# Kernel tuning notes

Hardware: AMD Instinct MI355X
Metric: run time of the kernel (lower is better)

The kernel has to match this reference:

```python
import jax, jax.numpy as jnp
import numpy as np

DIM = 2048
N_HEADS = 32
N_KV_HEADS = 8
HEAD_DIM = DIM // N_HEADS  # 64
N_REP = N_HEADS // N_KV_HEADS  # 4
ROPE_BASE = 10000.0


def _rope_cos_sin(seq_len, head_dim, dtype):
    inv_freq = 1.0 / (ROPE_BASE ** (jnp.arange(0, head_dim, 2, dtype=jnp.float32) / head_dim))
    freqs = jnp.arange(seq_len, dtype=jnp.float32)[:, None] * inv_freq[None, :]  # [S, hd/2]
    return jnp.cos(freqs).astype(dtype), jnp.sin(freqs).astype(dtype)


def _apply_rope(x, cos, sin):
    # x: [B, S, H, hd]; cos/sin: [S, hd/2]
    x1, x2 = jnp.split(x, 2, axis=-1)
    c = cos[None, :, None, :]
    s = sin[None, :, None, :]
    return jnp.concatenate([x1 * c - x2 * s, x1 * s + x2 * c], axis=-1)


def setup_inputs() -> dict:
    key = jax.random.key(0)
    ks = jax.random.split(key, 5)
    B, S = 2, 2048
    x = jax.random.normal(ks[0], (B, S, DIM), dtype=jnp.float32)
    scale = 1.0 / np.sqrt(DIM)
    wq = jax.random.normal(ks[1], (DIM, DIM), dtype=jnp.float32) * scale
    wk = jax.random.normal(ks[2], (N_KV_HEADS * HEAD_DIM, DIM), dtype=jnp.float32) * scale
    wv = jax.random.normal(ks[3], (N_KV_HEADS * HEAD_DIM, DIM), dtype=jnp.float32) * scale
    wo = jax.random.normal(ks[4], (DIM, DIM), dtype=jnp.float32) * scale
    return {"x": x, "wq": wq, "wk": wk, "wv": wv, "wo": wo}


def reference(x, wq, wk, wv, wo):
    B, S, D = x.shape
    # projections (nn.Linear: y = x @ W.T)
    xq = (x @ wq.T).reshape(B, S, N_HEADS, HEAD_DIM)
    xk = (x @ wk.T).reshape(B, S, N_KV_HEADS, HEAD_DIM)
    xv = (x @ wv.T).reshape(B, S, N_KV_HEADS, HEAD_DIM)

    cos, sin = _rope_cos_sin(S, HEAD_DIM, x.dtype)
    xq = _apply_rope(xq, cos, sin)
    xk = _apply_rope(xk, cos, sin)

    # GQA: repeat kv heads
    keys = jnp.repeat(xk, N_REP, axis=2)    # [B, S, H, hd]
    values = jnp.repeat(xv, N_REP, axis=2)

    scores = jnp.einsum('bqhd,bkhd->bhqk', xq, keys) / np.sqrt(HEAD_DIM)
    causal = jnp.tril(jnp.ones((S, S), dtype=bool))
    scores = jnp.where(causal[None, None, :, :], scores, jnp.finfo(scores.dtype).min)
    probs = jax.nn.softmax(scores, axis=-1)
    out = jnp.einsum('bhqk,bkhd->bqhd', probs, values).reshape(B, S, D)
    return out @ wo.T  # dropout in eval mode == identity
```

## Files before the change

kernel.cpp:

```cpp
#include <hip/hip_runtime.h>

typedef __attribute__((ext_vector_type(8))) short bf16x8;
typedef __attribute__((ext_vector_type(4))) float f32x4;
typedef __attribute__((ext_vector_type(4))) unsigned short u16x4;

#define GPTR(p) (const __attribute__((address_space(1))) void*)(p)
#define LPTR(p) (__attribute__((address_space(3))) void*)(p)

static __device__ __forceinline__ unsigned short f2bf(float f) {
  union { float f; unsigned int u; } x; x.f = f;
  unsigned int u = x.u;
  unsigned int r = (u + 0x7fffu + ((u >> 16) & 1u)) >> 16;
  return (unsigned short)r;
}
static __device__ __forceinline__ float bf2f(unsigned short h) {
  union { unsigned int u; float f; } x; x.u = ((unsigned int)h) << 16;
  return x.f;
}
static __device__ __forceinline__ f32x4 f32x4_zero() {
  f32x4 z = {0.f, 0.f, 0.f, 0.f}; return z;
}
static __device__ __forceinline__ unsigned int cvt_pk_bf16(float lo, float hi) {
  unsigned int r;
  asm("v_cvt_pk_bf16_f32 %0, %1, %2" : "=v"(r) : "v"(lo), "v"(hi));
  return r;
}

__global__ void rope_table_kernel(float* __restrict__ costab, float* __restrict__ sintab) {
  int i = blockIdx.x * blockDim.x + threadIdx.x;
  int s = i >> 5, d = i & 31;
  float invf = exp2f(-(float)d * (13.287712379549449f / 32.0f));
  float a = (float)s * invf;
  costab[i] = cosf(a);
  sintab[i] = sinf(a);
}

__global__ void f32_to_bf16(const float* __restrict__ src, unsigned short* __restrict__ dst, int n4) {
  int stride = gridDim.x * blockDim.x;
  for (int i = blockIdx.x * blockDim.x + threadIdx.x; i < n4; i += stride) {
    float4 v = ((const float4*)src)[i];
    u16x4 o;
    o.x = f2bf(v.x); o.y = f2bf(v.y); o.z = f2bf(v.z); o.w = f2bf(v.w);
    *(u16x4*)(dst + (size_t)i * 4) = o;
  }
}

template<int FM, int OUT_BF16>
__global__ __launch_bounds__(512, 2) void gemm8p(const unsigned short* __restrict__ A,
                                                 const unsigned short* __restrict__ B,
                                                 void* __restrict__ Cv,
                                                 int M, int N, int K, int nbx) {
  constexpr int BM = FM * 32;
  constexpr int MH = FM / 2;
  constexpr int ABYTES = BM * 128;
  constexpr int BBYTES = 256 * 128;
  __shared__ __align__(16) char lds_all[2 * ABYTES + 2 * BBYTES];
  char* lsA = lds_all;
  char* lsB = lds_all + 2 * ABYTES;

  const int tid = threadIdx.x;
  const int wave = tid >> 6, lane = tid & 63;
  const int fq = lane >> 4, fr = lane & 15;
  const int wr = wave >> 2, wc = wave & 3;

  const int nwg = gridDim.x;
  const int q8 = nwg >> 3;
  const int sw = (blockIdx.x & 7) * q8 + (blockIdx.x >> 3);
  const int by = sw / nbx;
  const int bx = sw - by * nbx;
  const int m0 = by * BM, n0 = bx * 256;

  const int arow = tid >> 3;
  const int scol = (((tid & 7) ^ (arow & 7)) << 4);

#define STAGE_A(bufv, kt, h)                                                                  \
  do {                                                                                        \
    const char* src_ = (const char*)A + ((size_t)(m0 + (h) * 128 + arow) * K + (kt) * 64) * 2 + scol; \
    char* dst_ = lsA + (bufv) * ABYTES + (h) * 16384 + tid * 16;                              \
    __builtin_amdgcn_global_load_lds(GPTR(src_), LPTR(dst_), 16, 0, 0);                       \
    __builtin_amdgcn_global_load_lds(GPTR(src_ + (size_t)64 * K * 2), LPTR(dst_ + 8192), 16, 0, 0); \
  } while (0)
#define STAGE_B(bufv, kt, h)                                                                  \
  do {                                                                                        \
    const char* src_ = (const char*)B + ((size_t)(n0 + (h) * 128 + arow) * K + (kt) * 64) * 2 + scol; \
    char* dst_ = lsB + (bufv) * BBYTES + (h) * 16384 + tid * 16;                              \
    __builtin_amdgcn_global_load_lds(GPTR(src_), LPTR(dst_), 16, 0, 0);                       \
    __builtin_amdgcn_global_load_lds(GPTR(src_ + (size_t)64 * K * 2), LPTR(dst_ + 8192), 16, 0, 0); \
  } while (0)

  f32x4 acc[FM][4];
#pragma unroll
  for (int i = 0; i < FM; ++i)
#pragma unroll
    for (int j = 0; j < 4; ++j) acc[i][j] = f32x4_zero();

#define PHASE(p)                                                                              \
  do {                                                                                        \
    constexpr int mh = (p) >> 1, nh = (p) & 1;                                                \
    bf16x8 af[MH][2], bfv[2][2];                                                              \
    _Pragma("unroll") for (int m = 0; m < MH; ++m) {                                          \
      const int rowA = wr * FM * 16 + mh * MH * 16 + m * 16 + fr;                             \
      const char* pa = lsA + buf * ABYTES + (rowA >> 7) * 16384 + (rowA & 127) * 128;         \
      const int sz = (rowA & 7) << 4;                                                         \
      af[m][0] = *(const bf16x8*)(pa + ((fq * 16) ^ sz));                                     \
      af[m][1] = *(const bf16x8*)(pa + ((64 + fq * 16) ^ sz));                                \
    }                                                                                         \
    _Pragma("unroll") for (int n = 0; n < 2; ++n) {                                           \
      const int rowB = wc * 64 + nh * 32 + n * 16 + fr;                                       \
      const char* pb = lsB + buf * BBYTES + (rowB >> 7) * 16384 + (rowB & 127) * 128;         \
      const int sz = (rowB & 7) << 4;                                                         \
      bfv[n][0] = *(const bf16x8*)(pb + ((fq * 16) ^ sz));                                    \
      bfv[n][1] = *(const bf16x8*)(pb + ((64 + fq * 16) ^ sz));                               \
    }                                                                                         \
    asm volatile("s_waitcnt lgkmcnt(0)" ::: "memory");                                        \
    __builtin_amdgcn_sched_barrier(0);                                                        \
    __builtin_amdgcn_s_setprio(1);                                                            \
    _Pragma("unroll") for (int m = 0; m < MH; ++m)                                            \
      _Pragma("unroll") for (int n = 0; n < 2; ++n) {                                         \
        acc[mh * MH + m][nh * 2 + n] =                                                        \
            __builtin_amdgcn_mfma_f32_16x16x32_bf16(af[m][0], bfv[n][0], acc[mh * MH + m][nh * 2 + n], 0, 0, 0); \
        acc[mh * MH + m][nh * 2 + n] =                                                        \
            __builtin_amdgcn_mfma_f32_16x16x32_bf16(af[m][1], bfv[n][1], acc[mh * MH + m][nh * 2 + n], 0, 0, 0); \
      }                                                                                       \
    __builtin_amdgcn_s_setprio(0);                                                            \
  } while (0)

  const int NT = K >> 6;

  STAGE_A(0, 0, 0);
  if constexpr (FM == 8) STAGE_A(0, 0, 1);
  STAGE_B(0, 0, 0);
  STAGE_B(0, 0, 1);
  asm volatile("s_waitcnt vmcnt(0)" ::: "memory");
  __builtin_amdgcn_s_barrier();

  int buf = 0;
  for (int t = 0; t < NT; ++t) {
    const bool hn = (t + 1) < NT;
    if (hn) {
      STAGE_A(buf ^ 1, t + 1, 0);
      asm volatile("s_waitcnt vmcnt(2)" ::: "memory");
    } else {
      asm volatile("s_waitcnt vmcnt(0)" ::: "memory");
    }
    __builtin_amdgcn_s_barrier();
    PHASE(0);
    __builtin_amdgcn_s_barrier();
    if (hn) {
      if constexpr (FM == 8) STAGE_A(buf ^ 1, t + 1, 1);
      else                   STAGE_B(buf ^ 1, t + 1, 0);
    }
    PHASE(1);
    __builtin_amdgcn_s_barrier();
    if (hn) {
      if constexpr (FM == 8) STAGE_B(buf ^ 1, t + 1, 0);
      else                   STAGE_B(buf ^ 1, t + 1, 1);
    }
    PHASE(2);
    __builtin_amdgcn_s_barrier();
    if (hn) {
      if constexpr (FM == 8) STAGE_B(buf ^ 1, t + 1, 1);
    }
    PHASE(3);
    __builtin_amdgcn_s_barrier();
    buf ^= 1;
  }

#pragma unroll
  for (int i = 0; i < FM; ++i) {
    const int row = m0 + wr * FM * 16 + i * 16 + fq * 4;
#pragma unroll
    for (int j = 0; j < 4; ++j) {
      const int col = n0 + wc * 64 + j * 16 + fr;
#pragma unroll
      for (int v = 0; v < 4; ++v) {
        if (OUT_BF16) ((unsigned short*)Cv)[(size_t)(row + v) * N + col] = f2bf(acc[i][j][v]);
        else          ((float*)Cv)[(size_t)(row + v) * N + col] = acc[i][j][v];
      }
    }
  }
#undef STAGE_A
#undef STAGE_B
#undef PHASE
}

__global__ void rope_kernel(unsigned short* __restrict__ qkv,
                            const float* __restrict__ costab,
                            const float* __restrict__ sintab) {
  int idx = blockIdx.x * blockDim.x + threadIdx.x;
  if (idx >= 4096 * 1280) return;
  int row = idx / 1280;
  int p = idx - row * 1280;
  int s = row & 2047;
  int col, d; bool isq;
  if (p < 1024) { isq = true;  d = p & 31; col = (p >> 5) * 64 + d; }
  else { isq = false; int pk = p - 1024; d = pk & 31; col = 2048 + (pk >> 5) * 64 + d; }
  float c = costab[s * 32 + d], sn = sintab[s * 32 + d];
  unsigned short* base = qkv + (size_t)row * 3072;
  float x1 = bf2f(base[col]), x2 = bf2f(base[col + 32]);
  float o1 = x1 * c - x2 * sn;
  float o2 = x1 * sn + x2 * c;
  if (isq) { o1 *= 0.18033688011112042f; o2 *= 0.18033688011112042f; }
  base[col] = f2bf(o1);
  base[col + 32] = f2bf(o2);
}

__global__ __launch_bounds__(512, 4) void flash_attn(const unsigned short* __restrict__ qkv,
                                                     unsigned short* __restrict__ out) {
  __shared__ __align__(16) char K_sh[2 * 8192];
  __shared__ __align__(16) char V_sh[2 * 8192];
  __shared__ __align__(16) char P_sh[8 * 4096];

  const int tid = threadIdx.x;
  const int wave = tid >> 6, lane = tid & 63;
  const int fq = lane >> 4, fr = lane & 15;
  const int id = blockIdx.x;
  const int w = id >> 8, c = id & 255;
  const int hb = c & 63;
  const int h = hb & 31, b = hb >> 5;
  const int qhalf = c >> 6;
  const int qt = w ? qhalf : 7 - qhalf;
  const int kvh = h >> 2;
  const int q0 = qt * 256;
  const int wq0 = q0 + wave * 32;
  char* Pw = P_sh + wave * 4096;

  bf16x8 qreg[2][2];
#pragma unroll
  for (int qf = 0; qf < 2; ++qf)
#pragma unroll
    for (int kk = 0; kk < 2; ++kk)
      qreg[qf][kk] = *(const bf16x8*)(qkv + (size_t)(b * 2048 + wq0 + qf * 16 + fr) * 3072
                                      + h * 64 + kk * 32 + fq * 8);

  f32x4 o_acc[4][2];
  float m_run[2], l_run[2];
#pragma unroll
  for (int dc = 0; dc < 4; ++dc) { o_acc[dc][0] = f32x4_zero(); o_acc[dc][1] = f32x4_zero(); }
  m_run[0] = m_run[1] = -1e30f;
  l_run[0] = l_run[1] = 0.f;

  const char* kgbase = (const char*)qkv + (size_t)(b * 2048) * 6144 + 4096 + kvh * 128;
  const unsigned short* vgbase = qkv + (size_t)(b * 2048) * 3072 + 2560 + kvh * 64;
  const int nsteps = (q0 + 256) >> 6;

  const int vk2 = (tid >> 3) << 1;
  const int vc0 = (tid & 7) << 3;
  const int kt = tid - 256;

  {
    if (wave < 4) {
      bf16x8 vv0 = *(const bf16x8*)(vgbase + (size_t)vk2 * 3072 + vc0);
      bf16x8 vv1 = *(const bf16x8*)(vgbase + (size_t)(vk2 + 1) * 3072 + vc0);
#pragma unroll
      for (int j = 0; j < 8; ++j) {
        const int d = vc0 + j;
        const int G = ((d & 7) ^ (d >> 3)) & 7;
        unsigned int w2 = ((unsigned int)(unsigned short)vv0[j]) |
                          (((unsigned int)(unsigned short)vv1[j]) << 16);
        *(unsigned int*)(V_sh + (d << 7) + ((vk2 << 1) ^ (G << 4))) = w2;
      }
    } else {
#pragma unroll
      for (int ld = 0; ld < 2; ++ld) {
        const int row = (kt >> 3) + (ld << 5);
        const int cb = ((kt & 7) << 4) ^ ((row & 7) << 4);
        __builtin_amdgcn_global_load_lds(GPTR(kgbase + (size_t)row * 6144 + cb),
                                         LPTR(K_sh + kt * 16 + ld * 4096), 16, 0, 0);
      }
    }
  }
  __syncthreads();

  int buf = 0;
  for (int st = 0; st < nsteps; ++st) {
    const int k0 = st << 6;
    const bool has_next = (st + 1) < nsteps;
    bf16x8 vv0, vv1;
    if (has_next) {
      const int k0n = k0 + 64;
      if (wave < 4) {
        vv0 = *(const bf16x8*)(vgbase + (size_t)(k0n + vk2) * 3072 + vc0);
        vv1 = *(const bf16x8*)(vgbase + (size_t)(k0n + vk2 + 1) * 3072 + vc0);
      } else {
        char* Kn = K_sh + (buf ^ 1) * 8192;
#pragma unroll
        for (int ld = 0; ld < 2; ++ld) {
          const int row = (kt >> 3) + (ld << 5);
          const int cb = ((kt & 7) << 4) ^ ((row & 7) << 4);
          __builtin_amdgcn_global_load_lds(GPTR(kgbase + (size_t)(k0n + row) * 6144 + cb),
                                           LPTR(Kn + kt * 16 + ld * 4096), 16, 0, 0);
        }
      }
    }

    if (k0 <= wq0 + 31) {
      const char* Kb = K_sh + buf * 8192;
      const char* Vb = V_sh + buf * 8192;
      f32x4 s[2][4];
#pragma unroll
      for (int qf = 0; qf < 2; ++qf)
#pragma unroll
        for (int kf = 0; kf < 4; ++kf) s[qf][kf] = f32x4_zero();
#pragma unroll
      for (int kf = 0; kf < 4; ++kf) {
        const int krow = kf * 16 + fr;
        const int swz = (krow & 7) << 4;
        bf16x8 ka = *(const bf16x8*)(Kb + krow * 128 + ((fq * 16) ^ swz));
        bf16x8 kb = *(const bf16x8*)(Kb + krow * 128 + ((64 + fq * 16) ^ swz));
#pragma unroll
        for (int qf = 0; qf < 2; ++qf) {
          s[qf][kf] = __builtin_amdgcn_mfma_f32_16x16x32_bf16(ka, qreg[qf][0], s[qf][kf], 0, 0, 0);
          s[qf][kf] = __builtin_amdgcn_mfma_f32_16x16x32_bf16(kb, qreg[qf][1], s[qf][kf], 0, 0, 0);
        }
      }
      if (k0 + 63 > wq0) {
#pragma unroll
        for (int qf = 0; qf < 2; ++qf) {
          const int q = wq0 + qf * 16 + fr;
#pragma unroll
          for (int kf = 0; kf < 4; ++kf)
#pragma unroll
            for (int v = 0; v < 4; ++v) {
              const int key = k0 + kf * 16 + fq * 4 + v;
              if (key > q) s[qf][kf][v] = -1e30f;
            }
        }
      }
#pragma unroll
      for (int qf = 0; qf < 2; ++qf) {
        float t = s[qf][0][0];
#pragma unroll
        for (int kf = 0; kf < 4; ++kf)
#pragma unroll
          for (int v = 0; v < 4; ++v) t = fmaxf(t, s[qf][kf][v]);
        t = fmaxf(t, __shfl_xor(t, 16));
        t = fmaxf(t, __shfl_xor(t, 32));
        const float mo = m_run[qf];
        const float mn = fmaxf(mo, t);
        const float sc = __builtin_amdgcn_exp2f(mo - mn);
        m_run[qf] = mn;
        float ps = 0.f;
#pragma unroll
        for (int kf = 0; kf < 4; ++kf)
#pragma unroll
          for (int v = 0; v < 4; ++v) {
            const float p = __builtin_amdgcn_exp2f(s[qf][kf][v] - mn);
            s[qf][kf][v] = p;
            ps += p;
          }
        ps += __shfl_xor(ps, 16);
        ps += __shfl_xor(ps, 32);
        l_run[qf] = l_run[qf] * sc + ps;
#pragma unroll
        for (int dc = 0; dc < 4; ++dc) o_acc[dc][qf] *= sc;
        const int r = qf * 16 + fr;
        const int rswz = (r & 7) << 4;
#pragma unroll
        for (int kf = 0; kf < 4; ++kf) {
          uint2 w2;
          w2.x = cvt_pk_bf16(s[qf][kf][0], s[qf][kf][1]);
          w2.y = cvt_pk_bf16(s[qf][kf][2], s[qf][kf][3]);
          *(uint2*)(Pw + r * 128 + ((kf * 32 + fq * 8) ^ rswz)) = w2;
        }
      }
      asm volatile("s_waitcnt lgkmcnt(0)" ::: "memory");
      __builtin_amdgcn_sched_barrier(0);
      const int fswz = (fr & 7) << 4;
#pragma unroll
      for (int kk = 0; kk < 2; ++kk) {
        bf16x8 pa0 = *(const bf16x8*)(Pw + fr * 128 + ((kk * 64 + fq * 16) ^ fswz));
        bf16x8 pa1 = *(const bf16x8*)(Pw + (16 + fr) * 128 + ((kk * 64 + fq * 16) ^ fswz));
#pragma unroll
        for (int dc = 0; dc < 4; ++dc) {
          const int d = dc * 16 + fr;
          const int G = ((d & 7) ^ (d >> 3)) & 7;
          bf16x8 vt = *(const bf16x8*)(Vb + d * 128 + ((kk * 64 + fq * 16) ^ (G << 4)));
          o_acc[dc][0] = __builtin_amdgcn_mfma_f32_16x16x32_bf16(vt, pa0, o_acc[dc][0], 0, 0, 0);
          o_acc[dc][1] = __builtin_amdgcn_mfma_f32_16x16x32_bf16(vt, pa1, o_acc[dc][1], 0, 0, 0);
        }
      }
    }

    if (has_next && wave < 4) {
      char* Vn = V_sh + (buf ^ 1) * 8192;
#pragma unroll
      for (int j = 0; j < 8; ++j) {
        const int d = vc0 + j;
        const int G = ((d & 7) ^ (d >> 3)) & 7;
        unsigned int w2 = ((unsigned int)(unsigned short)vv0[j]) |
                          (((unsigned int)(unsigned short)vv1[j]) << 16);
        *(unsigned int*)(Vn + (d << 7) + ((vk2 << 1) ^ (G << 4))) = w2;
      }
    }
    __syncthreads();
    buf ^= 1;
  }

#pragma unroll
  for (int qf = 0; qf < 2; ++qf) {
    const float inv = 1.0f / l_run[qf];
    const size_t row = (size_t)(b * 2048 + wq0 + qf * 16 + fr);
#pragma unroll
    for (int dc = 0; dc < 4; ++dc) {
      u16x4 o;
#pragma unroll
      for (int v = 0; v < 4; ++v) o[v] = f2bf(o_acc[dc][qf][v] * inv);
      *(u16x4*)(out + row * 2048 + h * 64 + dc * 16 + fq * 4) = o;
    }
  }
}

extern "C" void kernel_launch(void* const* d_in, const int* in_sizes, int n_in,
                              void* d_out, int out_size, void* d_ws, size_t ws_size,
                              hipStream_t stream) {
  (void)in_sizes; (void)n_in; (void)out_size; (void)ws_size;
  const float* x  = (const float*)d_in[0];
  const float* wq = (const float*)d_in[1];
  const float* wk = (const float*)d_in[2];
  const float* wv = (const float*)d_in[3];
  const float* wo = (const float*)d_in[4];

  char* wsb = (char*)d_ws;
  unsigned short* xb     = (unsigned short*)(wsb);
  unsigned short* attn_o = xb;
  unsigned short* wqkvb  = (unsigned short*)(wsb + 16777216);
  unsigned short* wob    = (unsigned short*)(wsb + 29360128);
  unsigned short* qkv    = (unsigned short*)(wsb + 37748736);
  float* costab          = (float*)(wsb + 62914560);
  float* sintab          = (float*)(wsb + 63176704);

  rope_table_kernel<<<256, 256, 0, stream>>>(costab, sintab);

  f32_to_bf16<<<2048, 256, 0, stream>>>(x,  xb,                 8388608 / 4);
  f32_to_bf16<<<1024, 256, 0, stream>>>(wq, wqkvb,              4194304 / 4);
  f32_to_bf16<<<256,  256, 0, stream>>>(wk, wqkvb + 4194304,    1048576 / 4);
  f32_to_bf16<<<256,  256, 0, stream>>>(wv, wqkvb + 5242880,    1048576 / 4);
  f32_to_bf16<<<1024, 256, 0, stream>>>(wo, wob,                4194304 / 4);

  gemm8p<8, 1><<<192, 512, 0, stream>>>(xb, wqkvb, (void*)qkv, 4096, 3072, 2048, 12);

  rope_kernel<<<20480, 256, 0, stream>>>(qkv, costab, sintab);

  flash_attn<<<512, 512, 0, stream>>>(qkv, attn_o);

  gemm8p<4, 0><<<256, 512, 0, stream>>>(attn_o, wob, d_out, 4096, 2048, 2048, 8);
}
```

Before: 288.7 us.

## Use lazy softmax rescaling, tree reductions, and reorder block-to-tile mapping

Online softmax now rescales the running max, sum and output accumulators only when some row's new max exceeds the old one by more than a threshold (checked wave-wide). This skips the per-tile exp and accumulator multiply in most iterations. Max and sum reductions are rewritten as balanced trees to shorten dependency chains. The block index mapping changes to put q-tiles innermost in descending order rather than the previous paired heavy/light interleave, which may change load balance across the causal triangle. Exponentials can reach up to about 2^11.5 before rescaling, which is safe in fp32 but trades some bf16 P precision.

```diff
diff --git a/kernel.cpp b/kernel.cpp
--- a/kernel.cpp
+++ b/kernel.cpp
@@ -215,11 +215,9 @@
   const int wave = tid >> 6, lane = tid & 63;
   const int fq = lane >> 4, fr = lane & 15;
   const int id = blockIdx.x;
-  const int w = id >> 8, c = id & 255;
-  const int hb = c & 63;
-  const int h = hb & 31, b = hb >> 5;
-  const int qhalf = c >> 6;
-  const int qt = w ? qhalf : 7 - qhalf;
+  const int qt = 7 - (id & 7);
+  const int h = (id >> 3) & 31;
+  const int b = id >> 8;
   const int kvh = h >> 2;
   const int q0 = qt * 256;
   const int wq0 = q0 + wave * 32;
@@ -327,33 +325,45 @@
             }
         }
       }
+      float pm[2];
 #pragma unroll
       for (int qf = 0; qf < 2; ++qf) {
-        float t = s[qf][0][0];
-#pragma unroll
-        for (int kf = 0; kf < 4; ++kf)
-#pragma unroll
-          for (int v = 0; v < 4; ++v) t = fmaxf(t, s[qf][kf][v]);
+        float a0 = fmaxf(fmaxf(s[qf][0][0], s[qf][0][1]), fmaxf(s[qf][0][2], s[qf][0][3]));
+        float a1 = fmaxf(fmaxf(s[qf][1][0], s[qf][1][1]), fmaxf(s[qf][1][2], s[qf][1][3]));
+        float a2 = fmaxf(fmaxf(s[qf][2][0], s[qf][2][1]), fmaxf(s[qf][2][2], s[qf][2][3]));
+        float a3 = fmaxf(fmaxf(s[qf][3][0], s[qf][3][1]), fmaxf(s[qf][3][2], s[qf][3][3]));
+        float t = fmaxf(fmaxf(a0, a1), fmaxf(a2, a3));
         t = fmaxf(t, __shfl_xor(t, 16));
         t = fmaxf(t, __shfl_xor(t, 32));
-        const float mo = m_run[qf];
-        const float mn = fmaxf(mo, t);
-        const float sc = __builtin_amdgcn_exp2f(mo - mn);
-        m_run[qf] = mn;
-        float ps = 0.f;
+        pm[qf] = t;
+      }
+      if (__any(fmaxf(pm[0] - m_run[0], pm[1] - m_run[1]) > 11.5f)) {
+#pragma unroll
+        for (int qf = 0; qf < 2; ++qf) {
+          const float mn = fmaxf(m_run[qf], pm[qf]);
+          const float sc = __builtin_amdgcn_exp2f(m_run[qf] - mn);
+          m_run[qf] = mn;
+          l_run[qf] *= sc;
+#pragma unroll
+          for (int dc = 0; dc < 4; ++dc) o_acc[dc][qf] *= sc;
+        }
+      }
+#pragma unroll
+      for (int qf = 0; qf < 2; ++qf) {
+        const float mn = m_run[qf];
 #pragma unroll
         for (int kf = 0; kf < 4; ++kf)
 #pragma unroll
-          for (int v = 0; v < 4; ++v) {
-            const float p = __builtin_amdgcn_exp2f(s[qf][kf][v] - mn);
-            s[qf][kf][v] = p;
-            ps += p;
-          }
+          for (int v = 0; v < 4; ++v)
+            s[qf][kf][v] = __builtin_amdgcn_exp2f(s[qf][kf][v] - mn);
+        float b0 = (s[qf][0][0] + s[qf][0][1]) + (s[qf][0][2] + s[qf][0][3]);
+        float b1 = (s[qf][1][0] + s[qf][1][1]) + (s[qf][1][2] + s[qf][1][3]);
+        float b2 = (s[qf][2][0] + s[qf][2][1]) + (s[qf][2][2] + s[qf][2][3]);
+        float b3 = (s[qf][3][0] + s[qf][3][1]) + (s[qf][3][2] + s[qf][3][3]);
+        float ps = (b0 + b1) + (b2 + b3);
         ps += __shfl_xor(ps, 16);
         ps += __shfl_xor(ps, 32);
-        l_run[qf] = l_run[qf] * sc + ps;
-#pragma unroll
-        for (int dc = 0; dc < 4; ++dc) o_acc[dc][qf] *= sc;
+        l_run[qf] += ps;
         const int r = qf * 16 + fr;
         const int rswz = (r & 7) << 4;
 #pragma unroll
```

After: 271.8 us. 5.9% less time.

## Keep attention probabilities in registers via lane permutes instead of LDS round-trip

Applied to the files above, without the earlier changes.

Drops the per-wave shared-memory P buffer. The softmax probabilities are now rearranged from the QK^T accumulator layout into the PV MFMA operand layout using permlane32_swap and xor-16 shuffles. This removes the LDS writes, the wait and the reads on every key tile, and frees 32KB of LDS, which may allow more resident blocks. It also changes the block-to-tile mapping to a plain qt/h/b decode, with causal tiles reversed so the heaviest run first.

```diff
diff --git a/kernel.cpp b/kernel.cpp
--- a/kernel.cpp
+++ b/kernel.cpp
@@ -3,6 +3,7 @@
 typedef __attribute__((ext_vector_type(8))) short bf16x8;
 typedef __attribute__((ext_vector_type(4))) float f32x4;
 typedef __attribute__((ext_vector_type(4))) unsigned short u16x4;
+typedef __attribute__((ext_vector_type(2))) unsigned int u32x2;
 
 #define GPTR(p) (const __attribute__((address_space(1))) void*)(p)
 #define LPTR(p) (__attribute__((address_space(3))) void*)(p)
@@ -209,21 +210,18 @@
                                                      unsigned short* __restrict__ out) {
   __shared__ __align__(16) char K_sh[2 * 8192];
   __shared__ __align__(16) char V_sh[2 * 8192];
-  __shared__ __align__(16) char P_sh[8 * 4096];
 
   const int tid = threadIdx.x;
   const int wave = tid >> 6, lane = tid & 63;
   const int fq = lane >> 4, fr = lane & 15;
+  const int q1 = fq & 1;
   const int id = blockIdx.x;
-  const int w = id >> 8, c = id & 255;
-  const int hb = c & 63;
-  const int h = hb & 31, b = hb >> 5;
-  const int qhalf = c >> 6;
-  const int qt = w ? qhalf : 7 - qhalf;
+  const int qt = 7 - (id & 7);
+  const int h = (id >> 3) & 31;
+  const int b = id >> 8;
   const int kvh = h >> 2;
   const int q0 = qt * 256;
   const int wq0 = q0 + wave * 32;
-  char* Pw = P_sh + wave * 4096;
 
   bf16x8 qreg[2][2];
 #pragma unroll
@@ -354,30 +352,37 @@
         l_run[qf] = l_run[qf] * sc + ps;
 #pragma unroll
         for (int dc = 0; dc < 4; ++dc) o_acc[dc][qf] *= sc;
-        const int r = qf * 16 + fr;
-        const int rswz = (r & 7) << 4;
-#pragma unroll
-        for (int kf = 0; kf < 4; ++kf) {
-          uint2 w2;
-          w2.x = cvt_pk_bf16(s[qf][kf][0], s[qf][kf][1]);
-          w2.y = cvt_pk_bf16(s[qf][kf][2], s[qf][kf][3]);
-          *(uint2*)(Pw + r * 128 + ((kf * 32 + fq * 8) ^ rswz)) = w2;
+      }
+#pragma unroll
+      for (int kk = 0; kk < 2; ++kk) {
+        bf16x8 pb[2];
+#pragma unroll
+        for (int qf = 0; qf < 2; ++qf) {
+          unsigned int u0w0 = cvt_pk_bf16(s[qf][2 * kk][0],     s[qf][2 * kk][1]);
+          unsigned int u0w1 = cvt_pk_bf16(s[qf][2 * kk][2],     s[qf][2 * kk][3]);
+          unsigned int u1w0 = cvt_pk_bf16(s[qf][2 * kk + 1][0], s[qf][2 * kk + 1][1]);
+          unsigned int u1w1 = cvt_pk_bf16(s[qf][2 * kk + 1][2], s[qf][2 * kk + 1][3]);
+          u32x2 s0 = __builtin_amdgcn_permlane32_swap(u0w0, u1w0, false, false);
+          u32x2 s1 = __builtin_amdgcn_permlane32_swap(u0w1, u1w1, false, false);
+          const unsigned int a0 = s0.x, b0 = s0.y, a1 = s1.x, b1 = s1.y;
+          const unsigned int ra0 = (unsigned int)__shfl_xor((int)a0, 16);
+          const unsigned int rb0 = (unsigned int)__shfl_xor((int)b0, 16);
+          const unsigned int ra1 = (unsigned int)__shfl_xor((int)a1, 16);
+          const unsigned int rb1 = (unsigned int)__shfl_xor((int)b1, 16);
+          union { unsigned int u[4]; bf16x8 v; } P;
+          P.u[0] = q1 ? rb0 : a0;
+          P.u[1] = q1 ? rb1 : a1;
+          P.u[2] = q1 ? b0 : ra0;
+          P.u[3] = q1 ? b1 : ra1;
+          pb[qf] = P.v;
         }
-      }
-      asm volatile("s_waitcnt lgkmcnt(0)" ::: "memory");
-      __builtin_amdgcn_sched_barrier(0);
-      const int fswz = (fr & 7) << 4;
-#pragma unroll
-      for (int kk = 0; kk < 2; ++kk) {
-        bf16x8 pa0 = *(const bf16x8*)(Pw + fr * 128 + ((kk * 64 + fq * 16) ^ fswz));
-        bf16x8 pa1 = *(const bf16x8*)(Pw + (16 + fr) * 128 + ((kk * 64 + fq * 16) ^ fswz));
 #pragma unroll
         for (int dc = 0; dc < 4; ++dc) {
           const int d = dc * 16 + fr;
           const int G = ((d & 7) ^ (d >> 3)) & 7;
           bf16x8 vt = *(const bf16x8*)(Vb + d * 128 + ((kk * 64 + fq * 16) ^ (G << 4)));
-          o_acc[dc][0] = __builtin_amdgcn_mfma_f32_16x16x32_bf16(vt, pa0, o_acc[dc][0], 0, 0, 0);
-          o_acc[dc][1] = __builtin_amdgcn_mfma_f32_16x16x32_bf16(vt, pa1, o_acc[dc][1], 0, 0, 0);
+          o_acc[dc][0] = __builtin_amdgcn_mfma_f32_16x16x32_bf16(vt, pb[0], o_acc[dc][0], 0, 0, 0);
+          o_acc[dc][1] = __builtin_amdgcn_mfma_f32_16x16x32_bf16(vt, pb[1], o_acc[dc][1], 0, 0, 0);
         }
       }
     }
```

After: 349.7 us. 1.21x slower.

## Fuse RoPE into QKV GEMM epilogue and merge conversion kernels

Applied to the files above, without the earlier changes.

Applies rotary embedding and the query scale directly in the QKV GEMM epilogue using an interleaved cos/sin table, which removes the separate rope kernel and its extra read-modify-write pass over qkv. The five fp32-to-bf16 conversion launches are merged into one kernel. The flash attention grid moves to a 3D layout with a plain reversed q-tile order, replacing the old balanced pairing of heavy and light tiles. The epilogue rounds to bf16 only once after rotation, which slightly changes numerics, and the new attention block order may change load balance.

```diff
diff --git a/kernel.cpp b/kernel.cpp
--- a/kernel.cpp
+++ b/kernel.cpp
@@ -26,30 +26,41 @@
   return r;
 }
 
-__global__ void rope_table_kernel(float* __restrict__ costab, float* __restrict__ sintab) {
+__global__ void rope_table_kernel(float2* __restrict__ ctab) {
   int i = blockIdx.x * blockDim.x + threadIdx.x;
   int s = i >> 5, d = i & 31;
   float invf = exp2f(-(float)d * (13.287712379549449f / 32.0f));
   float a = (float)s * invf;
-  costab[i] = cosf(a);
-  sintab[i] = sinf(a);
-}
-
-__global__ void f32_to_bf16(const float* __restrict__ src, unsigned short* __restrict__ dst, int n4) {
-  int stride = gridDim.x * blockDim.x;
-  for (int i = blockIdx.x * blockDim.x + threadIdx.x; i < n4; i += stride) {
-    float4 v = ((const float4*)src)[i];
+  ctab[i] = make_float2(cosf(a), sinf(a));
+}
+
+__global__ void convert_all(const float* __restrict__ x,  const float* __restrict__ wq,
+                            const float* __restrict__ wk, const float* __restrict__ wv,
+                            const float* __restrict__ wo,
+                            unsigned short* __restrict__ xb,
+                            unsigned short* __restrict__ wqkvb,
+                            unsigned short* __restrict__ wob) {
+  const int stride = gridDim.x * blockDim.x;
+  for (int i = blockIdx.x * blockDim.x + threadIdx.x; i < 4718592; i += stride) {
+    const float* src; unsigned short* dst; int off;
+    if (i < 2097152)      { src = x;  dst = xb;              off = i; }
+    else if (i < 3145728) { src = wq; dst = wqkvb;           off = i - 2097152; }
+    else if (i < 3407872) { src = wk; dst = wqkvb + 4194304; off = i - 3145728; }
+    else if (i < 3670016) { src = wv; dst = wqkvb + 5242880; off = i - 3407872; }
+    else                  { src = wo; dst = wob;             off = i - 3670016; }
+    float4 v = ((const float4*)src)[off];
     u16x4 o;
     o.x = f2bf(v.x); o.y = f2bf(v.y); o.z = f2bf(v.z); o.w = f2bf(v.w);
-    *(u16x4*)(dst + (size_t)i * 4) = o;
-  }
-}
-
-template<int FM, int OUT_BF16>
+    *(u16x4*)(dst + (size_t)off * 4) = o;
+  }
+}
+
+template<int FM, int OUT_BF16, int ROPE>
 __global__ __launch_bounds__(512, 2) void gemm8p(const unsigned short* __restrict__ A,
                                                  const unsigned short* __restrict__ B,
                                                  void* __restrict__ Cv,
-                                                 int M, int N, int K, int nbx) {
+                                                 int M, int N, int K, int nbx,
+                                                 const float2* __restrict__ ctab) {
   constexpr int BM = FM * 32;
   constexpr int MH = FM / 2;
   constexpr int ABYTES = BM * 128;
@@ -166,43 +177,51 @@
     buf ^= 1;
   }
 
-#pragma unroll
-  for (int i = 0; i < FM; ++i) {
-    const int row = m0 + wr * FM * 16 + i * 16 + fq * 4;
-#pragma unroll
-    for (int j = 0; j < 4; ++j) {
-      const int col = n0 + wc * 64 + j * 16 + fr;
-#pragma unroll
-      for (int v = 0; v < 4; ++v) {
-        if (OUT_BF16) ((unsigned short*)Cv)[(size_t)(row + v) * N + col] = f2bf(acc[i][j][v]);
-        else          ((float*)Cv)[(size_t)(row + v) * N + col] = acc[i][j][v];
+  if constexpr (ROPE) {
+    const int colbase = n0 + wc * 64 + fr;
+#pragma unroll
+    for (int i = 0; i < FM; ++i) {
+      const int row = m0 + wr * FM * 16 + i * 16 + fq * 4;
+      const int s0 = row & 2047;
+#pragma unroll
+      for (int j = 0; j < 2; ++j) {
+        const int col = colbase + j * 16;
+        const bool rot = col < 2560;
+        const float scale = (col < 2048) ? 0.18033688011112042f : 1.0f;
+        const int dp = col & 63;
+#pragma unroll
+        for (int v = 0; v < 4; ++v) {
+          const float a  = acc[i][j][v];
+          const float b2 = acc[i][j + 2][v];
+          float o1 = a, o2 = b2;
+          if (rot) {
+            const float2 cs = ctab[(s0 + v) * 32 + dp];
+            o1 = (a * cs.x - b2 * cs.y) * scale;
+            o2 = (a * cs.y + b2 * cs.x) * scale;
+          }
+          ((unsigned short*)Cv)[(size_t)(row + v) * N + col]      = f2bf(o1);
+          ((unsigned short*)Cv)[(size_t)(row + v) * N + col + 32] = f2bf(o2);
+        }
+      }
+    }
+  } else {
+#pragma unroll
+    for (int i = 0; i < FM; ++i) {
+      const int row = m0 + wr * FM * 16 + i * 16 + fq * 4;
+#pragma unroll
+      for (int j = 0; j < 4; ++j) {
+        const int col = n0 + wc * 64 + j * 16 + fr;
+#pragma unroll
+        for (int v = 0; v < 4; ++v) {
+          if (OUT_BF16) ((unsigned short*)Cv)[(size_t)(row + v) * N + col] = f2bf(acc[i][j][v]);
+          else          ((float*)Cv)[(size_t)(row + v) * N + col] = acc[i][j][v];
+        }
       }
     }
   }
 #undef STAGE_A
 #undef STAGE_B
 #undef PHASE
-}
-
-__global__ void rope_kernel(unsigned short* __restrict__ qkv,
-                            const float* __restrict__ costab,
-                            const float* __restrict__ sintab) {
-  int idx = blockIdx.x * blockDim.x + threadIdx.x;
-  if (idx >= 4096 * 1280) return;
-  int row = idx / 1280;
-  int p = idx - row * 1280;
-  int s = row & 2047;
-  int col, d; bool isq;
-  if (p < 1024) { isq = true;  d = p & 31; col = (p >> 5) * 64 + d; }
-  else { isq = false; int pk = p - 1024; d = pk & 31; col = 2048 + (pk >> 5) * 64 + d; }
-  float c = costab[s * 32 + d], sn = sintab[s * 32 + d];
-  unsigned short* base = qkv + (size_t)row * 3072;
-  float x1 = bf2f(base[col]), x2 = bf2f(base[col + 32]);
-  float o1 = x1 * c - x2 * sn;
-  float o2 = x1 * sn + x2 * c;
-  if (isq) { o1 *= 0.18033688011112042f; o2 *= 0.18033688011112042f; }
-  base[col] = f2bf(o1);
-  base[col + 32] = f2bf(o2);
 }
 
 __global__ __launch_bounds__(512, 4) void flash_attn(const unsigned short* __restrict__ qkv,
@@ -214,12 +233,8 @@
   const int tid = threadIdx.x;
   const int wave = tid >> 6, lane = tid & 63;
   const int fq = lane >> 4, fr = lane & 15;
-  const int id = blockIdx.x;
-  const int w = id >> 8, c = id & 255;
-  const int hb = c & 63;
-  const int h = hb & 31, b = hb >> 5;
-  const int qhalf = c >> 6;
-  const int qt = w ? qhalf : 7 - qhalf;
+  const int b = blockIdx.z, h = blockIdx.y;
+  const int qt = gridDim.x - 1 - blockIdx.x;
   const int kvh = h >> 2;
   const int q0 = qt * 256;
   const int wq0 = q0 + wave * 32;
@@ -427,22 +442,15 @@
   unsigned short* wqkvb  = (unsigned short*)(wsb + 16777216);
   unsigned short* wob    = (unsigned short*)(wsb + 29360128);
   unsigned short* qkv    = (unsigned short*)(wsb + 37748736);
-  float* costab          = (float*)(wsb + 62914560);
-  float* sintab          = (float*)(wsb + 63176704);
-
-  rope_table_kernel<<<256, 256, 0, stream>>>(costab, sintab);
-
-  f32_to_bf16<<<2048, 256, 0, stream>>>(x,  xb,                 8388608 / 4);
-  f32_to_bf16<<<1024, 256, 0, stream>>>(wq, wqkvb,              4194304 / 4);
-  f32_to_bf16<<<256,  256, 0, stream>>>(wk, wqkvb + 4194304,    1048576 / 4);
-  f32_to_bf16<<<256,  256, 0, stream>>>(wv, wqkvb + 5242880,    1048576 / 4);
-  f32_to_bf16<<<1024, 256, 0, stream>>>(wo, wob,                4194304 / 4);
-
-  gemm8p<8, 1><<<192, 512, 0, stream>>>(xb, wqkvb, (void*)qkv, 4096, 3072, 2048, 12);
-
-  rope_kernel<<<20480, 256, 0, stream>>>(qkv, costab, sintab);
-
-  flash_attn<<<512, 512, 0, stream>>>(qkv, attn_o);
-
-  gemm8p<4, 0><<<256, 512, 0, stream>>>(attn_o, wob, d_out, 4096, 2048, 2048, 8);
-}
+  float2* ctab           = (float2*)(wsb + 62914560);
+
+  rope_table_kernel<<<256, 256, 0, stream>>>(ctab);
+
+  convert_all<<<2048, 256, 0, stream>>>(x, wq, wk, wv, wo, xb, wqkvb, wob);
+
+  gemm8p<8, 1, 1><<<192, 512, 0, stream>>>(xb, wqkvb, (void*)qkv, 4096, 3072, 2048, 12, ctab);
+
+  flash_attn<<<dim3(8, 32, 2), 512, 0, stream>>>(qkv, attn_o);
+
+  gemm8p<4, 0, 0><<<256, 512, 0, stream>>>(attn_o, wob, d_out, 4096, 2048, 2048, 8, nullptr);
+}
```

Result: faster. 252.9 us (-12.4%).
